# Performance work log

Measured on AMD Instinct MI355X. Metric: run time of the kernel, lower is better.

The kernel has to match this reference:

```python
import jax, jax.numpy as jnp
import numpy as np

PRE_NMS_THRESH = 0.05
PRE_NMS_TOP_N = 1000
NMS_THRESH = 0.6
FPN_POST_NMS_TOP_N = 100
MIN_SIZE = 0
OFFSET = 10000.0  # per-class coordinate offset for batched per-class NMS
NEG = -1e9


def bilinear_resize(x, out_h, out_w):
    # x: [H, W, C] -> [out_h, out_w, C], matches torch interpolate(align_corners=False)
    H, W, _ = x.shape
    def grid(in_size, out_size):
        scale = in_size / out_size
        src = (jnp.arange(out_size, dtype=jnp.float32) + 0.5) * scale - 0.5
        src = jnp.clip(src, 0.0, in_size - 1.0)
        i0 = jnp.floor(src).astype(jnp.int32)
        i1 = jnp.minimum(i0 + 1, in_size - 1)
        lam = src - i0.astype(jnp.float32)
        return i0, i1, lam
    r0, r1, rl = grid(H, out_h)
    c0, c1, cl = grid(W, out_w)
    x = x[r0] * (1.0 - rl)[:, None, None] + x[r1] * rl[:, None, None]
    x = x[:, c0] * (1.0 - cl)[None, :, None] + x[:, c1] * cl[None, :, None]
    return x


def box_iou_plus1(b):
    area = (b[:, 2] - b[:, 0] + 1.0) * (b[:, 3] - b[:, 1] + 1.0)
    lt = jnp.maximum(b[:, None, :2], b[None, :, :2])
    rb = jnp.minimum(b[:, None, 2:], b[None, :, 2:])
    wh = jnp.clip(rb - lt + 1.0, 0.0)
    inter = wh[..., 0] * wh[..., 1]
    union = area[:, None] + area[None, :] - inter
    return inter / jnp.maximum(union, 1e-6)


def _forward(locations, box_cls, box_regression, centerness, box_mask, h, w):
    N, C, H, W = box_cls.shape
    M2 = box_mask.shape[1]
    Mi = int(np.sqrt(M2))
    HW = H * W
    K = PRE_NMS_TOP_N

    cls = jax.nn.sigmoid(box_cls.transpose(0, 2, 3, 1).reshape(N, HW, C))
    reg = box_regression.transpose(0, 2, 3, 1).reshape(N, HW, 4)
    cent = jax.nn.sigmoid(centerness.reshape(N, HW))
    mask = jax.nn.sigmoid(box_mask.transpose(0, 2, 3, 1))  # [N,H,W,M2]

    cand = cls > PRE_NMS_THRESH               # candidates from raw cls scores
    scr = cls * cent[:, :, None]              # centerness-weighted scores

    def per_image(cand_i, scr_i, reg_i, mask_i):
        # --- threshold + per-image topk (fixed K, padded with NEG) ---
        flat = jnp.where(cand_i, scr_i, NEG).reshape(HW * C)
        vals, idx = jax.lax.top_k(flat, K)
        valid = vals > NEG / 2
        loc_idx = idx // C
        labels = idx % C + 1                  # 1-based class labels
        locs = locations[loc_idx]             # [K,2]
        r = reg_i[loc_idx]                    # [K,4]
        boxes = jnp.stack([locs[:, 0] - r[:, 0], locs[:, 1] - r[:, 1],
                           locs[:, 0] + r[:, 2], locs[:, 1] + r[:, 3]], axis=1)
        scores = jnp.sqrt(jnp.where(valid, vals, 1.0)) * valid

        # --- mask paste: mean of upsampled mask over (buggy) box region ---
        up = bilinear_resize(mask_i, h, w)                      # [h,w,M2]
        integ = jnp.pad(jnp.cumsum(jnp.cumsum(up, 0), 1), ((1, 0), (1, 0), (0, 0)))
        bi = boxes.astype(jnp.int32)          # torch .int() truncation
        x1 = jnp.maximum(bi[:, 0], 0); x2 = jnp.minimum(bi[:, 2], h - 1)
        y1 = jnp.maximum(bi[:, 1], 0); y2 = jnp.minimum(bi[:, 3], w - 1)
        # original skip condition is (x1>=x2 or y1>=x2) -- bug replicated; extra
        # y1<y2 guard avoids NaN mean over empty region
        region_ok = (x1 < x2) & (y1 < x2) & (y1 < y2)
        x1c = jnp.clip(x1, 0, h); x2c = jnp.clip(x2, 0, h)
        y1c = jnp.clip(y1, 0, w); y2c = jnp.clip(y2, 0, w)
        s = integ[x2c, y2c] - integ[x1c, y2c] - integ[x2c, y1c] + integ[x1c, y1c]
        area = jnp.maximum((x2c - x1c) * (y2c - y1c), 1).astype(s.dtype)
        prob = ((s / area[:, None]) * region_ok[:, None]).reshape(K, Mi, Mi)

        # --- clip_to_image (x in [0,w-1], y in [0,h-1]) + remove_small_boxes ---
        bx = jnp.stack([jnp.clip(boxes[:, 0], 0, w - 1), jnp.clip(boxes[:, 1], 0, h - 1),
                        jnp.clip(boxes[:, 2], 0, w - 1), jnp.clip(boxes[:, 3], 0, h - 1)], 1)
        ws_ = bx[:, 2] - bx[:, 0] + 1.0
        hs_ = bx[:, 3] - bx[:, 1] + 1.0
        valid = valid & (ws_ >= MIN_SIZE) & (hs_ >= MIN_SIZE)

        # --- per-class greedy NMS via class-offset trick (fixed shape) ---
        nb = bx + (labels.astype(bx.dtype) * OFFSET)[:, None]
        order = jnp.argsort(-jnp.where(valid, scores, -1.0))
        nb_s, sc_s, v_s = nb[order], scores[order], valid[order]
        iou = box_iou_plus1(nb_s)
        rng = jnp.arange(K)
        def step(keep, i):
            ki = keep[i] & v_s[i]
            keep = keep.at[i].set(ki)
            keep = keep & ~(ki & (iou[i] > NMS_THRESH) & (rng > i))
            return keep, None
        keep, _ = jax.lax.scan(step, jnp.ones(K, bool), jnp.arange(K))
        v_final = keep & v_s

        # --- keep fpn_post_nms_top_n highest-scoring survivors ---
        fvals, fidx = jax.lax.top_k(jnp.where(v_final, sc_s, -1.0), FPN_POST_NMS_TOP_N)
        sel = order[fidx]
        vfin = v_final[fidx]
        return (bx[sel], scores[sel] * vfin, labels[sel], prob[sel] * vfin[:, None, None], vfin)

    return jax.vmap(per_image)(cand, scr, reg, mask)


def setup_inputs() -> dict:
    key = jax.random.key(0)
    ks = jax.random.split(key, 4)
    N, C, H, W, M2 = 2, 80, 32, 40, 196
    stride = 8
    ys, xs = jnp.meshgrid(jnp.arange(H), jnp.arange(W), indexing='ij')
    locations = jnp.stack([xs.reshape(-1), ys.reshape(-1)], 1).astype(jnp.float32) * stride + stride // 2
    box_cls = jax.random.normal(ks[0], (N, C, H, W), jnp.float32) - 2.0
    box_regression = jax.random.uniform(ks[1], (N, 4, H, W), jnp.float32) * 60.0 + 4.0
    centerness = jax.random.normal(ks[2], (N, 1, H, W), jnp.float32)
    box_mask = jax.random.normal(ks[3], (N, M2, H, W), jnp.float32)
    return {"locations": locations, "box_cls": box_cls, "box_regression": box_regression,
            "centerness": centerness, "box_mask": box_mask, "image_h": 256, "image_w": 320}


def reference(locations, box_cls, box_regression, centerness, box_mask, image_h, image_w):
    return _forward(locations, box_cls, box_regression, centerness, box_mask, image_h, image_w)
```

## Files before the change

### kernel.cpp

```cpp
#include <hip/hip_runtime.h>

#define DEVI __device__ __forceinline__

constexpr int N_ = 2, C_ = 80, H_ = 32, W_ = 40, HW_ = H_ * W_, HWC_ = HW_ * C_;
constexpr int KTOP = 1000, M2_ = 196;
constexpr int IMH = 256, IMW = 320;
constexpr int BUFCAP = 4096;
constexpr int NB = 2048;
constexpr int KB = 16;
constexpr int SLICE = HWC_ / KB;

constexpr int O_SC = 800, O_LB = 1000, O_PB = 1200, O_VF = 40400;

DEVI unsigned long long mapd(double v) {
  unsigned long long u = (unsigned long long)__double_as_longlong(v);
  return (u & 0x8000000000000000ull) ? ~u : (u | 0x8000000000000000ull);
}
DEVI double unmapd(unsigned long long k) {
  unsigned long long u = (k & 0x8000000000000000ull) ? (k ^ 0x8000000000000000ull) : ~k;
  return __longlong_as_double((long long)u);
}
DEVI int i0of(int x, int cap) {
  float src = ((float)x + 0.5f) * 0.125f - 0.5f;
  src = fminf(fmaxf(src, 0.f), (float)cap);
  return (int)floorf(src);
}

__global__ __launch_bounds__(1024) void k_pre(const float* cls, const float* cent, const float* bm,
                                              unsigned* ghist, unsigned* cand,
                                              float* msig, float* wr, float* wc) {
  int b = blockIdx.x, tid = threadIdx.x;
  if (b < N_ * KB) {
    __shared__ unsigned hist[NB];
    __shared__ unsigned run[NB];
    __shared__ unsigned short binls[SLICE];
    __shared__ float ce[HW_];
    __shared__ unsigned wtot[16], wabove[16];
    int n = b / KB, sb = b % KB;
    size_t base = (size_t)n * HWC_ + (size_t)sb * SLICE;
    for (int j = tid; j < NB; j += 1024) hist[j] = 0;
    for (int j = tid; j < HW_; j += 1024) ce[j] = 1.f / (1.f + expf(-cent[n * HW_ + j]));
    __syncthreads();
    #pragma unroll
    for (int it = 0; it < 7; ++it) {
      int j = it * 1024 + tid;
      if (j < SLICE) {
        float a = cls[base + j];
        float s = 1.f / (1.f + expf(-a));
        unsigned short bb = 0xFFFF;
        if (s > 0.0499999f) {
          float key = s * ce[j % HW_];
          unsigned kb2 = __float_as_uint(key);
          int bin = (int)(kb2 >> 16) - 0x3800;
          bin = bin < 0 ? 0 : (bin > NB - 1 ? NB - 1 : bin);
          bb = (unsigned short)bin;
          atomicAdd(&hist[bin], 1u);
        }
        binls[j] = bb;
      }
    }
    __syncthreads();
    unsigned* gh = ghist + ((size_t)n * KB + sb) * NB;
    for (int j = tid; j < NB; j += 1024) gh[j] = hist[j];
    int lane = tid & 63, wid = tid >> 6;
    unsigned aa = hist[2 * tid], bv = hist[2 * tid + 1];
    unsigned s2 = aa + bv, suf = s2;
    for (int off = 1; off < 64; off <<= 1) {
      unsigned v = __shfl_down(suf, off);
      if (lane + off < 64) suf += v;
    }
    if (lane == 0) wtot[wid] = suf;
    __syncthreads();
    if (tid == 0) { unsigned acc = 0; for (int w = 15; w >= 0; --w) { wabove[w] = acc; acc += wtot[w]; } }
    __syncthreads();
    unsigned above = (suf - s2) + wabove[wid];
    run[2 * tid + 1] = above;
    run[2 * tid] = above + bv;
    __syncthreads();
    unsigned* ca = cand + ((size_t)n * KB + sb) * SLICE;
    #pragma unroll
    for (int it = 0; it < 7; ++it) {
      int j = it * 1024 + tid;
      if (j < SLICE) {
        unsigned short bb = binls[j];
        if (bb != 0xFFFF) {
          unsigned pos = atomicAdd(&run[bb], 1u);
          ca[pos] = (unsigned)(base + j);
        }
      }
    }
  } else if (b < N_ * KB + 140) {
    __shared__ float tile[4][32][33];
    int g = tid >> 8, sub = tid & 255;
    int tt = (b - N_ * KB) * 4 + g;
    int n = tt / 280, r = tt % 280, rqt = r / 7, ct = r % 7;
    int tx = sub & 31, ty = sub >> 5;
    int rq0 = rqt * 32, c0 = ct * 32;
    for (int i = 0; i < 4; ++i) {
      int cc = c0 + ty + i * 8, rq = rq0 + tx;
      if (cc < M2_) {
        float v = bm[((size_t)n * M2_ + cc) * HW_ + rq];
        tile[g][ty + i * 8][tx] = 1.f / (1.f + expf(-v));
      }
    }
    __syncthreads();
    for (int i = 0; i < 4; ++i) {
      int rq = rq0 + ty + i * 8, cc = c0 + tx;
      if (cc < M2_) msig[((size_t)n * HW_ + rq) * M2_ + cc] = tile[g][tx][ty + i * 8];
    }
  } else {
    int t = tid;
    if (t < H_) {
      int r = t; float acc = 0.f; wr[0 * H_ + r] = 0.f;
      for (int x = 0; x < IMH; ++x) {
        float src = ((float)x + 0.5f) * ((float)H_ / (float)IMH) - 0.5f;
        src = fminf(fmaxf(src, 0.f), (float)(H_ - 1));
        int i0 = (int)floorf(src); int i1 = min(i0 + 1, H_ - 1);
        float lam = src - (float)i0;
        float w = ((r == i0) ? (1.f - lam) : 0.f) + ((r == i1) ? lam : 0.f);
        acc += w; wr[(x + 1) * H_ + r] = acc;
      }
    } else if (t < H_ + W_) {
      int q = t - H_; float acc = 0.f; wc[0 * W_ + q] = 0.f;
      for (int y = 0; y < IMW; ++y) {
        float src = ((float)y + 0.5f) * ((float)W_ / (float)IMW) - 0.5f;
        src = fminf(fmaxf(src, 0.f), (float)(W_ - 1));
        int i0 = (int)floorf(src); int i1 = min(i0 + 1, W_ - 1);
        float lam = src - (float)i0;
        float w = ((q == i0) ? (1.f - lam) : 0.f) + ((q == i1) ? lam : 0.f);
        acc += w; wc[(y + 1) * W_ + q] = acc;
      }
    }
  }
}

struct SortSh { unsigned long long K[BUFCAP]; unsigned I[BUFCAP]; };

__global__ __launch_bounds__(1024) void k_sel(const unsigned* ghist, const unsigned* cand,
                                              const float* cls, const float* cent,
                                              const float* loc, const float* breg,
                                              double* bxd, double* scd, int* lab, int* vld, int* rg,
                                              unsigned* keepg) {
  __shared__ SortSh sh;
  __shared__ unsigned wtot[16], wabove[16], sliceCnt[16], sliceOff[17];
  __shared__ unsigned sD;
  int n = blockIdx.x, tid = threadIdx.x, lane = tid & 63, wid = tid >> 6;
  keepg[n * 1024 + tid] = 0;
  const unsigned* gh = ghist + (size_t)n * KB * NB;
  unsigned a = 0, bv = 0;
  #pragma unroll
  for (int q = 0; q < KB; ++q) { a += gh[q * NB + 2 * tid]; bv += gh[q * NB + 2 * tid + 1]; }
  if (tid == 0) sD = 0;
  unsigned s2 = a + bv, suf = s2;
  for (int off = 1; off < 64; off <<= 1) {
    unsigned v = __shfl_down(suf, off);
    if (lane + off < 64) suf += v;
  }
  if (lane == 0) wtot[wid] = suf;
  __syncthreads();
  if (tid == 0) { unsigned acc = 0; for (int w = 15; w >= 0; --w) { wabove[w] = acc; acc += wtot[w]; } }
  __syncthreads();
  unsigned above = (suf - s2) + wabove[wid];
  if (above < 1000u && above + bv >= 1000u) sD = (unsigned)(2 * tid + 1);
  if (above + bv < 1000u && above + bv + a >= 1000u) sD = (unsigned)(2 * tid);
  __syncthreads();
  unsigned D = sD;
  unsigned Dg = (D > 0) ? D - 1 : 0;
  {
    unsigned acc = 0;
    for (int bin = (int)Dg + lane; bin < NB; bin += 64) acc += gh[wid * NB + bin];
    for (int off = 32; off; off >>= 1) acc += __shfl_down(acc, off);
    if (lane == 0) sliceCnt[wid] = acc;
  }
  __syncthreads();
  if (tid == 0) {
    unsigned acc = 0;
    for (int q = 0; q < KB; ++q) { sliceOff[q] = acc; acc += sliceCnt[q]; }
    sliceOff[KB] = acc;
  }
  __syncthreads();
  int G = (int)sliceOff[KB]; if (G > BUFCAP) G = BUFCAP;
  {
    const unsigned* ca = cand + ((size_t)n * KB + wid) * SLICE;
    unsigned cs = sliceCnt[wid], so = sliceOff[wid];
    for (unsigned e = lane; e < cs; e += 64) {
      unsigned pos = so + e;
      if (pos < (unsigned)BUFCAP) {
        unsigned t = ca[e];
        int c = (int)((t % (unsigned)HWC_) / (unsigned)HW_);
        int hw = (int)(t % (unsigned)HW_);
        double aa = (double)cls[t];
        double ss = 1.0 / (1.0 + exp(-aa));
        double ced = 1.0 / (1.0 + exp(-(double)cent[n * HW_ + hw]));
        double v = (ss > 0.05) ? ss * ced : -1e9;
        sh.K[pos] = mapd(v);
        sh.I[pos] = (unsigned)(hw * C_ + c);
      }
    }
  }
  __syncthreads();
  int P = 1024; while (P < G) P <<= 1;
  for (int j = G + tid; j < P; j += 1024) { sh.K[j] = 0ull; sh.I[j] = 0xFFFFFFFFu; }
  __syncthreads();
  int E = P >> 10;
  for (int sz = 2; sz <= P; sz <<= 1) {
    for (int st = sz >> 1; st >= 64; st >>= 1) {
      for (int p = tid; p < (P >> 1); p += 1024) {
        int i = ((p & ~(st - 1)) << 1) | (p & (st - 1));
        int j = i | st;
        bool up = ((i & sz) == 0);
        unsigned long long k1 = sh.K[i], k2 = sh.K[j];
        unsigned i1 = sh.I[i], i2 = sh.I[j];
        bool bef = (k1 > k2) || (k1 == k2 && i1 < i2);
        if (bef != up) { sh.K[i] = k2; sh.K[j] = k1; sh.I[i] = i2; sh.I[j] = i1; }
      }
      __syncthreads();
    }
    {
      int st0 = ((sz >> 1) < 32) ? (sz >> 1) : 32;
      for (int e = 0; e < E; ++e) {
        int elem = tid + (e << 10);
        unsigned long long k = sh.K[elem];
        unsigned ii = sh.I[elem];
        bool dir = ((elem & sz) == 0);
        for (int st = st0; st >= 1; st >>= 1) {
          unsigned long long ko = __shfl_xor(k, st);
          unsigned io = __shfl_xor(ii, st);
          bool low = ((elem & st) == 0);
          bool first = (k > ko) || (k == ko && ii < io);
          bool take_mine = first ^ (!low) ^ (!dir);
          if (!take_mine) { k = ko; ii = io; }
        }
        sh.K[elem] = k; sh.I[elem] = ii;
      }
      __syncthreads();
    }
  }

  if (tid < KTOP) {
    unsigned long long key = sh.K[tid];
    unsigned idx = sh.I[tid];
    double v = unmapd(key);
    int valid = (v > -5e8) && (idx < (unsigned)HWC_);
    if (idx >= (unsigned)HWC_) idx = 0;
    int hw = (int)(idx / C_), c = (int)(idx % C_);
    double lx = (double)loc[hw * 2 + 0], ly = (double)loc[hw * 2 + 1];
    const float* rg4 = breg + (size_t)n * 4 * HW_;
    double r0 = (double)rg4[0 * HW_ + hw], r1 = (double)rg4[1 * HW_ + hw];
    double r2 = (double)rg4[2 * HW_ + hw], r3 = (double)rg4[3 * HW_ + hw];
    double b0 = lx - r0, b1 = ly - r1, b2 = lx + r2, b3 = ly + r3;
    double sc = valid ? sqrt(v) : 0.0;
    int bi0 = (int)b0, bi1 = (int)b1, bi2 = (int)b2, bi3 = (int)b3;
    int x1 = max(bi0, 0), x2 = min(bi2, IMH - 1), y1 = max(bi1, 0), y2 = min(bi3, IMW - 1);
    int rok = (x1 < x2) && (y1 < x2) && (y1 < y2);
    int x1c = min(max(x1, 0), IMH), x2c = min(max(x2, 0), IMH);
    int y1c = min(max(y1, 0), IMW), y2c = min(max(y2, 0), IMW);
    int area = max((x2c - x1c) * (y2c - y1c), 1);
    double c0 = fmin(fmax(b0, 0.0), (double)(IMW - 1));
    double c1 = fmin(fmax(b1, 0.0), (double)(IMH - 1));
    double c2 = fmin(fmax(b2, 0.0), (double)(IMW - 1));
    double c3 = fmin(fmax(b3, 0.0), (double)(IMH - 1));
    size_t base = (size_t)n * 1024 + tid;
    bxd[base * 4 + 0] = c0; bxd[base * 4 + 1] = c1; bxd[base * 4 + 2] = c2; bxd[base * 4 + 3] = c3;
    scd[base] = sc; lab[base] = c + 1; vld[base] = valid;
    int* r8 = rg + base * 8;
    r8[0] = x1c; r8[1] = x2c; r8[2] = y1c; r8[3] = y2c; r8[4] = area; r8[5] = rok;
  }
}

__global__ void k_nms(const double* bxd, const int* lab, const int* vld, unsigned* keepg) {
  int cls = blockIdx.x + 1, n = blockIdx.y, tid = threadIdx.x;
  __shared__ int mk[KTOP];
  __shared__ double mb0[KTOP], mb1[KTOP], mb2[KTOP], mb3[KTOP], ma[KTOP];
  __shared__ unsigned char kept[KTOP];
  int m = 0;
  for (int base = 0; base < KTOP; base += 64) {
    int t = base + tid;
    bool pred = (t < KTOP) && (lab[n * 1024 + t] == cls) && (vld[n * 1024 + t] != 0);
    unsigned long long bb = __ballot(pred);
    if (pred) {
      int pos = m + (int)__popcll(bb & ((1ull << tid) - 1ull));
      mk[pos] = t;
      const double* p = bxd + ((size_t)n * 1024 + t) * 4;
      double b0 = p[0], b1 = p[1], b2 = p[2], b3 = p[3];
      mb0[pos] = b0; mb1[pos] = b1; mb2[pos] = b2; mb3[pos] = b3;
      ma[pos] = (b2 - b0 + 1.0) * (b3 - b1 + 1.0);
      kept[pos] = 1;
    }
    m += (int)__popcll(bb);
  }
  __syncthreads();
  for (int i = 0; i < m; ++i) {
    if (kept[i]) {
      double x1 = mb0[i], y1 = mb1[i], x2 = mb2[i], y2 = mb3[i], ai = ma[i];
      for (int j = i + 1 + tid; j < m; j += 64) {
        double ltx = fmax(x1, mb0[j]), lty = fmax(y1, mb1[j]);
        double rbx = fmin(x2, mb2[j]), rby = fmin(y2, mb3[j]);
        double iw = fmax(rbx - ltx + 1.0, 0.0), ih = fmax(rby - lty + 1.0, 0.0);
        double inter = iw * ih;
        double uni = ai + ma[j] - inter;
        if (inter / fmax(uni, 1e-6) > 0.6) kept[j] = 0;
      }
    }
    __syncthreads();
  }
  for (int i = tid; i < m; i += 64) keepg[n * 1024 + mk[i]] = (unsigned)kept[i];
}

__global__ __launch_bounds__(256) void k_finish(const unsigned* keepg, const double* bxd,
                                                const double* scd, const int* lab, const int* rg,
                                                const float* msig, const float* wr, const float* wc,
                                                float* out) {
  int t = blockIdx.x, n = blockIdx.y, tid = threadIdx.x, lane = tid & 63, wid = tid >> 6;
  __shared__ int lsel[100], lvf[100];
  __shared__ unsigned woff[4]; __shared__ unsigned sS;
  __shared__ float A[H_], B[W_];

  int i0 = tid * 4;
  unsigned ff[4]; int lc = 0;
  for (int j = 0; j < 4; ++j) {
    int i = i0 + j;
    ff[j] = (i < KTOP) ? keepg[n * 1024 + i] : 0u;
    lc += (int)ff[j];
  }
  unsigned pre = (unsigned)lc;
  for (int off = 1; off < 64; off <<= 1) {
    unsigned v = __shfl_up(pre, off);
    if (lane >= off) pre += v;
  }
  if (lane == 63) woff[wid] = pre;
  __syncthreads();
  if (tid == 0) { unsigned acc = 0; for (int w = 0; w < 4; ++w) { unsigned tmp = woff[w]; woff[w] = acc; acc += tmp; } sS = acc; }
  __syncthreads();
  int kpre = (int)(woff[wid] + pre - (unsigned)lc);
  int S = (int)sS;
  for (int j = 0; j < 4; ++j) {
    int i = i0 + j;
    if (i < KTOP) {
      if (ff[j]) { if (kpre < 100) { lsel[kpre] = i; lvf[kpre] = 1; } kpre++; }
      else { int slot = S + (i - kpre); if (slot < 100) { lsel[slot] = i; lvf[slot] = 0; } }
    }
  }
  __syncthreads();

  int k = lsel[t], vf = lvf[t];
  if (tid == 0) {
    const double* bb = bxd + ((size_t)n * 1024 + k) * 4;
    out[(n * 100 + t) * 4 + 0] = (float)bb[0];
    out[(n * 100 + t) * 4 + 1] = (float)bb[1];
    out[(n * 100 + t) * 4 + 2] = (float)bb[2];
    out[(n * 100 + t) * 4 + 3] = (float)bb[3];
    out[O_SC + n * 100 + t] = vf ? (float)scd[n * 1024 + k] : 0.f;
    out[O_LB + n * 100 + t] = (float)lab[n * 1024 + k];
    out[O_VF + n * 100 + t] = (float)vf;
  }
  const int* r8 = rg + ((size_t)n * 1024 + k) * 8;
  int x1c = r8[0], x2c = r8[1], y1c = r8[2], y2c = r8[3], area = r8[4], rok = r8[5];
  if (tid < H_) A[tid] = wr[x2c * H_ + tid] - wr[x1c * H_ + tid];
  else if (tid < H_ + W_) { int q = tid - H_; B[q] = wc[y2c * W_ + q] - wc[y1c * W_ + q]; }
  __syncthreads();
  if (tid < M2_) {
    float acc = 0.f;
    if (rok && vf) {
      int rlo = i0of(x1c, H_ - 1);
      int rhi = min(i0of(x2c - 1, H_ - 1) + 1, H_ - 1);
      int qlo = i0of(y1c, W_ - 1);
      int qhi = min(i0of(y2c - 1, W_ - 1) + 1, W_ - 1);
      for (int r = rlo; r <= rhi; ++r) {
        float ar = A[r];
        const float* mrow = msig + ((size_t)((n * H_ + r) * W_ + qlo)) * M2_ + tid;
        float rs = 0.f;
        #pragma unroll 4
        for (int q = qlo; q <= qhi; ++q) { rs += B[q] * mrow[0]; mrow += M2_; }
        acc += ar * rs;
      }
      acc /= (float)area;
    }
    out[O_PB + (size_t)(n * 100 + t) * M2_ + tid] = acc;
  }
}

extern "C" void kernel_launch(void* const* d_in, const int* in_sizes, int n_in,
                              void* d_out, int out_size, void* d_ws, size_t ws_size,
                              hipStream_t stream) {
  (void)in_sizes; (void)n_in; (void)out_size; (void)ws_size;
  const float* locations = (const float*)d_in[0];
  const float* box_cls   = (const float*)d_in[1];
  const float* box_reg   = (const float*)d_in[2];
  const float* cent      = (const float*)d_in[3];
  const float* box_mask  = (const float*)d_in[4];
  float* out = (float*)d_out;

  char* ws = (char*)d_ws;
  size_t off = 0;
  auto alloc = [&](size_t bytes) -> void* {
    void* p = ws + off;
    off = (off + bytes + 255) & ~(size_t)255;
    return p;
  };
  unsigned* ghist = (unsigned*)alloc((size_t)N_ * KB * NB * 4);
  unsigned* cand  = (unsigned*)alloc((size_t)N_ * KB * SLICE * 4);
  double* bxd     = (double*)alloc((size_t)N_ * 1024 * 4 * 8);
  double* scd     = (double*)alloc((size_t)N_ * 1024 * 8);
  int* lab        = (int*)alloc((size_t)N_ * 1024 * 4);
  int* vld        = (int*)alloc((size_t)N_ * 1024 * 4);
  int* rg         = (int*)alloc((size_t)N_ * 1024 * 8 * 4);
  unsigned* keepg = (unsigned*)alloc((size_t)N_ * 1024 * 4);
  float* msig     = (float*)alloc((size_t)N_ * HW_ * M2_ * 4);
  float* wr       = (float*)alloc((size_t)(IMH + 1) * H_ * 4);
  float* wc       = (float*)alloc((size_t)(IMW + 1) * W_ * 4);

  k_pre<<<N_ * KB + 140 + 1, 1024, 0, stream>>>(box_cls, cent, box_mask, ghist, cand, msig, wr, wc);
  k_sel<<<N_, 1024, 0, stream>>>(ghist, cand, box_cls, cent, locations, box_reg,
                                 bxd, scd, lab, vld, rg, keepg);
  k_nms<<<dim3(C_, N_), 64, 0, stream>>>(bxd, lab, vld, keepg);
  k_finish<<<dim3(100, N_), 256, 0, stream>>>(keepg, bxd, scd, lab, rg, msig, wr, wc, out);
}
```

Measured before the change: 100.9 us.

## Replace candidate scatter with rescan-and-ballot compaction in selection kernel

Removes the per-slice prefix scan and bin-ordered candidate scatter from the histogram kernel, along with the global candidate buffer. The selection kernel now recomputes sigmoid scores over the full class map for its image. It compacts entries whose bin is at or above the threshold bin into shared memory using wave ballots and a shared atomic counter. This trades global writes and reads plus extra syncs in the first kernel for a full serial rescan done by only one block per image.

New measurement: 138.0 us. 1.37x slower.

```diff
diff --git a/kernel.cpp b/kernel.cpp
--- a/kernel.cpp
+++ b/kernel.cpp
@@ -5,10 +5,10 @@
 constexpr int N_ = 2, C_ = 80, H_ = 32, W_ = 40, HW_ = H_ * W_, HWC_ = HW_ * C_;
 constexpr int KTOP = 1000, M2_ = 196;
 constexpr int IMH = 256, IMW = 320;
-constexpr int BUFCAP = 4096;
 constexpr int NB = 2048;
 constexpr int KB = 16;
 constexpr int SLICE = HWC_ / KB;
+constexpr int BCAP = 4096;
 
 constexpr int O_SC = 800, O_LB = 1000, O_PB = 1200, O_VF = 40400;
 
@@ -27,16 +27,12 @@
 }
 
 __global__ __launch_bounds__(1024) void k_pre(const float* cls, const float* cent, const float* bm,
-                                              unsigned* ghist, unsigned* cand,
-                                              float* msig, float* wr, float* wc) {
+                                              unsigned* ghist, float* msig, float* wr, float* wc) {
   int b = blockIdx.x, tid = threadIdx.x;
   if (b < N_ * KB) {
     __shared__ unsigned hist[NB];
-    __shared__ unsigned run[NB];
-    __shared__ unsigned short binls[SLICE];
     __shared__ float ce[HW_];
-    __shared__ unsigned wtot[16], wabove[16];
-    int n = b / KB, sb = b % KB;
+    int n = b >> 4, sb = b & 15;
     size_t base = (size_t)n * HWC_ + (size_t)sb * SLICE;
     for (int j = tid; j < NB; j += 1024) hist[j] = 0;
     for (int j = tid; j < HW_; j += 1024) ce[j] = 1.f / (1.f + expf(-cent[n * HW_ + j]));
@@ -45,50 +41,19 @@
     for (int it = 0; it < 7; ++it) {
       int j = it * 1024 + tid;
       if (j < SLICE) {
-        float a = cls[base + j];
-        float s = 1.f / (1.f + expf(-a));
-        unsigned short bb = 0xFFFF;
+        float aa = cls[base + j];
+        float s = 1.f / (1.f + expf(-aa));
         if (s > 0.0499999f) {
-          float key = s * ce[j % HW_];
-          unsigned kb2 = __float_as_uint(key);
-          int bin = (int)(kb2 >> 16) - 0x3800;
+          unsigned key = __float_as_uint(s * ce[j % HW_]);
+          int bin = (int)(key >> 16) - 0x3800;
           bin = bin < 0 ? 0 : (bin > NB - 1 ? NB - 1 : bin);
-          bb = (unsigned short)bin;
           atomicAdd(&hist[bin], 1u);
         }
-        binls[j] = bb;
       }
     }
     __syncthreads();
     unsigned* gh = ghist + ((size_t)n * KB + sb) * NB;
     for (int j = tid; j < NB; j += 1024) gh[j] = hist[j];
-    int lane = tid & 63, wid = tid >> 6;
-    unsigned aa = hist[2 * tid], bv = hist[2 * tid + 1];
-    unsigned s2 = aa + bv, suf = s2;
-    for (int off = 1; off < 64; off <<= 1) {
-      unsigned v = __shfl_down(suf, off);
-      if (lane + off < 64) suf += v;
-    }
-    if (lane == 0) wtot[wid] = suf;
-    __syncthreads();
-    if (tid == 0) { unsigned acc = 0; for (int w = 15; w >= 0; --w) { wabove[w] = acc; acc += wtot[w]; } }
-    __syncthreads();
-    unsigned above = (suf - s2) + wabove[wid];
-    run[2 * tid + 1] = above;
-    run[2 * tid] = above + bv;
-    __syncthreads();
-    unsigned* ca = cand + ((size_t)n * KB + sb) * SLICE;
-    #pragma unroll
-    for (int it = 0; it < 7; ++it) {
-      int j = it * 1024 + tid;
-      if (j < SLICE) {
-        unsigned short bb = binls[j];
-        if (bb != 0xFFFF) {
-          unsigned pos = atomicAdd(&run[bb], 1u);
-          ca[pos] = (unsigned)(base + j);
-        }
-      }
-    }
   } else if (b < N_ * KB + 140) {
     __shared__ float tile[4][32][33];
     int g = tid >> 8, sub = tid & 255;
@@ -134,23 +99,24 @@
   }
 }
 
-struct SortSh { unsigned long long K[BUFCAP]; unsigned I[BUFCAP]; };
-
-__global__ __launch_bounds__(1024) void k_sel(const unsigned* ghist, const unsigned* cand,
-                                              const float* cls, const float* cent,
-                                              const float* loc, const float* breg,
-                                              double* bxd, double* scd, int* lab, int* vld, int* rg,
-                                              unsigned* keepg) {
+struct SortSh { unsigned long long K[BCAP]; unsigned I[BCAP]; };
+
+__global__ __launch_bounds__(1024) void k_seldec(const unsigned* ghist, const float* cls,
+                                                 const float* cent, const float* loc, const float* breg,
+                                                 double* bxd, double* scd, int* lab, int* vld, int* rg,
+                                                 unsigned* keepg) {
   __shared__ SortSh sh;
-  __shared__ unsigned wtot[16], wabove[16], sliceCnt[16], sliceOff[17];
-  __shared__ unsigned sD;
+  __shared__ float ce[HW_];
+  __shared__ unsigned wtot[16], wabove[16];
+  __shared__ unsigned sD, sCnt;
   int n = blockIdx.x, tid = threadIdx.x, lane = tid & 63, wid = tid >> 6;
   keepg[n * 1024 + tid] = 0;
+  for (int j = tid; j < HW_; j += 1024) ce[j] = 1.f / (1.f + expf(-cent[n * HW_ + j]));
   const unsigned* gh = ghist + (size_t)n * KB * NB;
   unsigned a = 0, bv = 0;
   #pragma unroll
   for (int q = 0; q < KB; ++q) { a += gh[q * NB + 2 * tid]; bv += gh[q * NB + 2 * tid + 1]; }
-  if (tid == 0) sD = 0;
+  if (tid == 0) { sD = 0; sCnt = 0; }
   unsigned s2 = a + bv, suf = s2;
   for (int off = 1; off < 64; off <<= 1) {
     unsigned v = __shfl_down(suf, off);
@@ -165,40 +131,44 @@
   if (above + bv < 1000u && above + bv + a >= 1000u) sD = (unsigned)(2 * tid);
   __syncthreads();
   unsigned D = sD;
-  unsigned Dg = (D > 0) ? D - 1 : 0;
-  {
-    unsigned acc = 0;
-    for (int bin = (int)Dg + lane; bin < NB; bin += 64) acc += gh[wid * NB + bin];
-    for (int off = 32; off; off >>= 1) acc += __shfl_down(acc, off);
-    if (lane == 0) sliceCnt[wid] = acc;
-  }
-  __syncthreads();
-  if (tid == 0) {
-    unsigned acc = 0;
-    for (int q = 0; q < KB; ++q) { sliceOff[q] = acc; acc += sliceCnt[q]; }
-    sliceOff[KB] = acc;
-  }
-  __syncthreads();
-  int G = (int)sliceOff[KB]; if (G > BUFCAP) G = BUFCAP;
-  {
-    const unsigned* ca = cand + ((size_t)n * KB + wid) * SLICE;
-    unsigned cs = sliceCnt[wid], so = sliceOff[wid];
-    for (unsigned e = lane; e < cs; e += 64) {
-      unsigned pos = so + e;
-      if (pos < (unsigned)BUFCAP) {
-        unsigned t = ca[e];
-        int c = (int)((t % (unsigned)HWC_) / (unsigned)HW_);
-        int hw = (int)(t % (unsigned)HW_);
-        double aa = (double)cls[t];
-        double ss = 1.0 / (1.0 + exp(-aa));
-        double ced = 1.0 / (1.0 + exp(-(double)cent[n * HW_ + hw]));
-        double v = (ss > 0.05) ? ss * ced : -1e9;
-        sh.K[pos] = mapd(v);
-        sh.I[pos] = (unsigned)(hw * C_ + c);
-      }
-    }
-  }
-  __syncthreads();
+  int Dg = (D > 0) ? (int)D - 1 : 0;
+
+  const float* cb = cls + (size_t)n * HWC_;
+  for (int it = 0; it < HWC_ / 1024; ++it) {
+    int j = it * 1024 + tid;
+    float aa = cb[j];
+    float s = 1.f / (1.f + expf(-aa));
+    bool win = false;
+    if (s > 0.0499999f) {
+      unsigned key = __float_as_uint(s * ce[j % HW_]);
+      int bin = (int)(key >> 16) - 0x3800;
+      bin = bin < 0 ? 0 : (bin > NB - 1 ? NB - 1 : bin);
+      win = (bin >= Dg);
+    }
+    unsigned long long mb = __ballot(win);
+    if (mb) {
+      int lead = __builtin_ctzll(mb);
+      unsigned offw = 0;
+      if (lane == lead) offw = atomicAdd(&sCnt, (unsigned)__popcll(mb));
+      offw = (unsigned)__shfl((int)offw, lead);
+      if (win) {
+        unsigned pos = offw + (unsigned)__popcll(mb & ((1ull << lane) - 1ull));
+        if (pos < (unsigned)BCAP)
+          sh.I[pos] = (unsigned)((j % HW_) * C_ + j / HW_);
+      }
+    }
+  }
+  __syncthreads();
+  int G = (int)sCnt; if (G > BCAP) G = BCAP;
+  for (int pos = tid; pos < G; pos += 1024) {
+    unsigned idx = sh.I[pos];
+    int hw = (int)(idx / C_), c = (int)(idx % C_);
+    double aa = (double)cls[(size_t)n * HWC_ + (size_t)c * HW_ + hw];
+    double ss = 1.0 / (1.0 + exp(-aa));
+    double ced = 1.0 / (1.0 + exp(-(double)cent[n * HW_ + hw]));
+    double v = (ss > 0.05) ? ss * ced : -1e9;
+    sh.K[pos] = mapd(v);
+  }
   int P = 1024; while (P < G) P <<= 1;
   for (int j = G + tid; j < P; j += 1024) { sh.K[j] = 0ull; sh.I[j] = 0xFFFFFFFFu; }
   __syncthreads();
@@ -236,7 +206,6 @@
       __syncthreads();
     }
   }
-
   if (tid < KTOP) {
     unsigned long long key = sh.K[tid];
     unsigned idx = sh.I[tid];
@@ -399,7 +368,6 @@
     return p;
   };
   unsigned* ghist = (unsigned*)alloc((size_t)N_ * KB * NB * 4);
-  unsigned* cand  = (unsigned*)alloc((size_t)N_ * KB * SLICE * 4);
   double* bxd     = (double*)alloc((size_t)N_ * 1024 * 4 * 8);
   double* scd     = (double*)alloc((size_t)N_ * 1024 * 8);
   int* lab        = (int*)alloc((size_t)N_ * 1024 * 4);
@@ -410,9 +378,9 @@
   float* wr       = (float*)alloc((size_t)(IMH + 1) * H_ * 4);
   float* wc       = (float*)alloc((size_t)(IMW + 1) * W_ * 4);
 
-  k_pre<<<N_ * KB + 140 + 1, 1024, 0, stream>>>(box_cls, cent, box_mask, ghist, cand, msig, wr, wc);
-  k_sel<<<N_, 1024, 0, stream>>>(ghist, cand, box_cls, cent, locations, box_reg,
-                                 bxd, scd, lab, vld, rg, keepg);
+  k_pre<<<N_ * KB + 140 + 1, 1024, 0, stream>>>(box_cls, cent, box_mask, ghist, msig, wr, wc);
+  k_seldec<<<N_, 1024, 0, stream>>>(ghist, box_cls, cent, locations, box_reg,
+                                    bxd, scd, lab, vld, rg, keepg);
   k_nms<<<dim3(C_, N_), 64, 0, stream>>>(bxd, lab, vld, keepg);
   k_finish<<<dim3(100, N_), 256, 0, stream>>>(keepg, bxd, scd, lab, rg, msig, wr, wc, out);
 }
```
